# Performance work log

Hardware: AMD Instinct MI355X
Metric: run time of the kernel (lower is better)

The kernel has to match this reference:

```python
import jax, jax.numpy as jnp
import numpy as np

N_ENT = 200000
N_REL = 500
D_MODEL = 512
BS = 256


def setup_inputs() -> dict:
    key = jax.random.key(0)
    k1, k2, k3, k4, k5, k6 = jax.random.split(key, 6)
    return {
        "s_ent": jax.random.randint(k1, (BS,), 0, N_ENT, dtype=jnp.int32),
        "relation": jax.random.randint(k2, (BS,), 0, N_REL, dtype=jnp.int32),
        "o_ent": jax.random.randint(k3, (BS,), 0, N_ENT, dtype=jnp.int32),
        "time": jax.random.randint(k4, (BS,), 0, 365, dtype=jnp.int32),
        "ent_emb": jax.random.normal(k5, (N_ENT, D_MODEL), dtype=jnp.float32),
        "rel_emb": jax.random.normal(k6, (N_REL, D_MODEL), dtype=jnp.float32),
    }


def reference(s_ent, relation, o_ent, time, ent_emb, rel_emb):
    # test_forward: scores = -||(e_s + r) - E_all||_2 for every entity.
    # Faithful math via the ||a-b||^2 = ||a||^2 - 2 a.b + ||b||^2 GEMM
    # decomposition, avoiding the [bs, n_ent, d] difference tensor.
    cond = ent_emb[s_ent] + rel_emb[relation]          # [bs, d]
    a2 = jnp.sum(cond * cond, axis=-1, keepdims=True)  # [bs, 1]
    b2 = jnp.sum(ent_emb * ent_emb, axis=-1)           # [n_ent]
    ab = jnp.einsum('bd,nd->bn', cond, ent_emb)        # [bs, n_ent]
    d2 = a2 - 2.0 * ab + b2[None, :]
    scores = -jnp.sqrt(jnp.maximum(d2, 1e-12))
    return scores
```

## Files before the change

kernel.cpp:

```cpp
#include <hip/hip_runtime.h>
#include <hip/hip_bf16.h>

typedef __attribute__((ext_vector_type(8))) short short8;
typedef __attribute__((ext_vector_type(4))) float f32x4;

#define D_MODEL 512
#define BN 128
#define NT 16
#define A_TILE 16384
#define B_TILE 8192

__device__ __forceinline__ void gload16(const void* g, void* l) {
    typedef const __attribute__((address_space(1))) unsigned GT;
    typedef __attribute__((address_space(3))) unsigned LT;
    __builtin_amdgcn_global_load_lds((GT*)g, (LT*)l, 16, 0, 0);
}

__device__ __forceinline__ short f2bf(float f) {
    unsigned u = __builtin_bit_cast(unsigned, f);
    unsigned r = (u + 0x7fffu + ((u >> 16) & 1u)) >> 16;
    return (short)r;
}

__device__ __forceinline__ short8 cvt8(const float4& a, const float4& b) {
    union { __hip_bfloat162 h[4]; short8 s; } u;
    u.h[0] = __float22bfloat162_rn(make_float2(a.x, a.y));
    u.h[1] = __float22bfloat162_rn(make_float2(a.z, a.w));
    u.h[2] = __float22bfloat162_rn(make_float2(b.x, b.y));
    u.h[3] = __float22bfloat162_rn(make_float2(b.z, b.w));
    return u.s;
}
__device__ __forceinline__ float ssq(const float4& a, const float4& b) {
    return a.x*a.x + a.y*a.y + a.z*a.z + a.w*a.w
         + b.x*b.x + b.y*b.y + b.z*b.z + b.w*b.w;
}

__global__ void prep_kernel(const int* __restrict__ s_ent, const int* __restrict__ rel,
                            const float* __restrict__ ent, const float* __restrict__ relemb,
                            short* __restrict__ condb, float* __restrict__ a2) {
    const int b = blockIdx.x;
    const int t = threadIdx.x;
    const float4 v = *(const float4*)(ent + (size_t)s_ent[b] * D_MODEL + t * 4);
    const float4 w = *(const float4*)(relemb + (size_t)rel[b] * D_MODEL + t * 4);
    float c0 = v.x + w.x, c1 = v.y + w.y, c2 = v.z + w.z, c3 = v.w + w.w;
    float sq = c0 * c0 + c1 * c1 + c2 * c2 + c3 * c3;

    short4 s;
    s.x = f2bf(c0); s.y = f2bf(c1); s.z = f2bf(c2); s.w = f2bf(c3);
    *(short4*)(condb + (size_t)b * D_MODEL + t * 4) = s;

    #pragma unroll
    for (int off = 1; off < 64; off <<= 1) sq += __shfl_xor(sq, off);
    __shared__ float red[2];
    if ((t & 63) == 0) red[t >> 6] = sq;
    __syncthreads();
    if (t == 0) a2[b] = red[0] + red[1];
}

__global__ __launch_bounds__(512, 4)
void score_kernel(const float* __restrict__ ent, const short* __restrict__ condb,
                  const float* __restrict__ a2, float* __restrict__ out, const int n_ent) {
    __shared__ __align__(16) unsigned char lds[2 * A_TILE + 2 * B_TILE];
    unsigned char* Al = lds;
    unsigned char* Bl = lds + 2 * A_TILE;

    const int tid  = threadIdx.x;
    const int lane = tid & 63;
    const int w    = tid >> 6, wm = w >> 1, wn = w & 1;
    const int lrow = lane & 15, g4 = lane >> 4;
    const int nbase = blockIdx.x * BN;

    const int p0 = tid * 16, p1 = p0 + 8192;
    const int ar0 = p0 >> 6, ar1 = p1 >> 6;
    const char* gA0 = (const char*)condb + ar0 * 1024 + ((p0 & 63) ^ ((ar0 & 3) << 4));
    const char* gA1 = (const char*)condb + ar1 * 1024 + ((p1 & 63) ^ ((ar1 & 3) << 4));

    const int sr = tid >> 2, sk = (tid & 3) * 8;
    const long long gr = min((long long)(nbase + sr), (long long)(n_ent - 1));
    const float* gB = ent + gr * D_MODEL + sk;
    const int bwoff = sr * 64 + ((sk * 2) ^ ((sr & 3) << 4));

    const int base_a = (wm * 64 + lrow) * 64 + ((g4 * 16) ^ ((lrow & 3) << 4));
    const int base_b = (wn * 64 + lrow) * 64 + ((g4 * 16) ^ ((lrow & 3) << 4));

    f32x4 acc[4][4] = {};
    float sq = 0.f;

    float4 rbA0 = *(const float4*)(gB);
    float4 rbA1 = *(const float4*)(gB + 4);
    float4 rbB0 = *(const float4*)(gB + 32);
    float4 rbB1 = *(const float4*)(gB + 36);
    gload16(gA0, Al + p0);
    gload16(gA1, Al + p1);
    sq += ssq(rbA0, rbA1);
    *(short8*)(Bl + bwoff) = cvt8(rbA0, rbA1);

#define KSTEP(T, CV0, CV1, LD0, LD1, DO_CVT, DO_LDB, DO_LDA)                              \
  {                                                                                        \
    asm volatile("s_waitcnt vmcnt(0)" ::: "memory");                                       \
    short8 cb;                                                                             \
    if (DO_CVT) { sq += ssq(CV0, CV1); cb = cvt8(CV0, CV1); }                              \
    asm volatile("s_waitcnt lgkmcnt(0)" ::: "memory");                                     \
    __builtin_amdgcn_s_barrier();                                                          \
    if (DO_LDB) { LD0 = *(const float4*)(gB + ((T) + 2) * 32);                             \
                  LD1 = *(const float4*)(gB + ((T) + 2) * 32 + 4); }                       \
    if (DO_LDA) { unsigned char* ad = Al + (((T) + 1) & 1) * A_TILE;                       \
                  gload16(gA0 + ((T) + 1) * 64, ad + p0);                                  \
                  gload16(gA1 + ((T) + 1) * 64, ad + p1); }                                \
    if (DO_CVT) *(short8*)(Bl + (((T) + 1) & 1) * B_TILE + bwoff) = cb;                    \
    const unsigned char* ab = Al + ((T) & 1) * A_TILE;                                     \
    const unsigned char* bb = Bl + ((T) & 1) * B_TILE;                                     \
    short8 af0 = *(const short8*)(ab + base_a);                                            \
    short8 af1 = *(const short8*)(ab + base_a + 1024);                                     \
    short8 af2 = *(const short8*)(ab + base_a + 2048);                                     \
    short8 af3 = *(const short8*)(ab + base_a + 3072);                                     \
    _Pragma("unroll")                                                                      \
    for (int fn = 0; fn < 4; ++fn) {                                                       \
      short8 bf = *(const short8*)(bb + base_b + fn * 1024);                               \
      acc[0][fn] = __builtin_amdgcn_mfma_f32_16x16x32_bf16(af0, bf, acc[0][fn], 0, 0, 0);  \
      acc[1][fn] = __builtin_amdgcn_mfma_f32_16x16x32_bf16(af1, bf, acc[1][fn], 0, 0, 0);  \
      acc[2][fn] = __builtin_amdgcn_mfma_f32_16x16x32_bf16(af2, bf, acc[2][fn], 0, 0, 0);  \
      acc[3][fn] = __builtin_amdgcn_mfma_f32_16x16x32_bf16(af3, bf, acc[3][fn], 0, 0, 0);  \
    }                                                                                      \
  }

    for (int tt = 0; tt < 14; tt += 2) {
        KSTEP(tt,     rbB0, rbB1, rbA0, rbA1, true,  true,  true)
        KSTEP(tt + 1, rbA0, rbA1, rbB0, rbB1, true,  true,  true)
    }
    KSTEP(14, rbB0, rbB1, rbA0, rbA1, true,  false, true)
    KSTEP(15, rbA0, rbA1, rbB0, rbB1, false, false, false)
#undef KSTEP

    sq += __shfl_xor(sq, 1);
    sq += __shfl_xor(sq, 2);
    float* b2s = (float*)lds;
    if ((tid & 3) == 0) b2s[sr] = sq;
    __syncthreads();

    #pragma unroll
    for (int fm = 0; fm < 4; ++fm) {
        const int m0 = wm * 64 + fm * 16 + g4 * 4;
        const f32x4 a2v = *(const f32x4*)(a2 + m0);
        #pragma unroll
        for (int fn = 0; fn < 4; ++fn) {
            const int nl = wn * 64 + fn * 16 + lrow;
            const int ng = nbase + nl;
            if (ng < n_ent) {
                const float b2v = b2s[nl];
                #pragma unroll
                for (int r = 0; r < 4; ++r) {
                    float d2 = a2v[r] - 2.f * acc[fm][fn][r] + b2v;
                    out[(size_t)(m0 + r) * n_ent + ng] = -sqrtf(fmaxf(d2, 1e-12f));
                }
            }
        }
    }
}

extern "C" void kernel_launch(void* const* d_in, const int* in_sizes, int n_in,
                              void* d_out, int out_size, void* d_ws, size_t ws_size,
                              hipStream_t stream) {
    const int*   s_ent  = (const int*)d_in[0];
    const int*   rel    = (const int*)d_in[1];
    const float* ent    = (const float*)d_in[4];
    const float* relemb = (const float*)d_in[5];
    float* out = (float*)d_out;

    const int bs    = in_sizes[0];
    const int n_ent = in_sizes[4] / D_MODEL;

    short* condb = (short*)d_ws;
    float* a2    = (float*)((char*)d_ws + (size_t)bs * D_MODEL * 2);

    prep_kernel<<<bs, 128, 0, stream>>>(s_ent, rel, ent, relemb, condb, a2);

    const int ntiles = (n_ent + BN - 1) / BN;
    score_kernel<<<ntiles, 512, 0, stream>>>(ent, condb, a2, out, n_ent);
}
```

Baseline: 173.7 us.

## Deepen score kernel to triple-buffered pipeline with partial vmcnt waits and setprio

Switches the GEMM K-loop from double to triple buffering in LDS, with global loads issued two steps ahead. Waits now use partial vmcnt counts instead of draining all loads, so memory latency can overlap more compute. MFMA sections are wrapped in s_setprio to favour math issue. LDS per block grows, which may reduce the number of resident blocks per CU.

```diff
diff --git a/kernel.cpp b/kernel.cpp
--- a/kernel.cpp
+++ b/kernel.cpp
@@ -60,9 +60,9 @@
 __global__ __launch_bounds__(512, 4)
 void score_kernel(const float* __restrict__ ent, const short* __restrict__ condb,
                   const float* __restrict__ a2, float* __restrict__ out, const int n_ent) {
-    __shared__ __align__(16) unsigned char lds[2 * A_TILE + 2 * B_TILE];
+    __shared__ __align__(16) unsigned char lds[3 * A_TILE + 3 * B_TILE];
     unsigned char* Al = lds;
-    unsigned char* Bl = lds + 2 * A_TILE;
+    unsigned char* Bl = lds + 3 * A_TILE;
 
     const int tid  = threadIdx.x;
     const int lane = tid & 63;
@@ -86,34 +86,41 @@
     f32x4 acc[4][4] = {};
     float sq = 0.f;
 
-    float4 rbA0 = *(const float4*)(gB);
-    float4 rbA1 = *(const float4*)(gB + 4);
-    float4 rbB0 = *(const float4*)(gB + 32);
-    float4 rbB1 = *(const float4*)(gB + 36);
+    float4 rbE0 = *(const float4*)(gB);
+    float4 rbE1 = *(const float4*)(gB + 4);
+    asm volatile("s_waitcnt vmcnt(0)" ::: "memory");
+    sq += ssq(rbE0, rbE1);
+    *(short8*)(Bl + bwoff) = cvt8(rbE0, rbE1);
+    float4 rbO0 = *(const float4*)(gB + 32);
+    float4 rbO1 = *(const float4*)(gB + 36);
     gload16(gA0, Al + p0);
     gload16(gA1, Al + p1);
-    sq += ssq(rbA0, rbA1);
-    *(short8*)(Bl + bwoff) = cvt8(rbA0, rbA1);
+    rbE0 = *(const float4*)(gB + 64);
+    rbE1 = *(const float4*)(gB + 68);
+    gload16(gA0 + 64, Al + A_TILE + p0);
+    gload16(gA1 + 64, Al + A_TILE + p1);
 
-#define KSTEP(T, CV0, CV1, LD0, LD1, DO_CVT, DO_LDB, DO_LDA)                              \
+#define KSTEP(T, CV0, CV1, DO_CVT, DO_B, DO_A, VM)                                        \
   {                                                                                        \
-    asm volatile("s_waitcnt vmcnt(0)" ::: "memory");                                       \
-    short8 cb;                                                                             \
-    if (DO_CVT) { sq += ssq(CV0, CV1); cb = cvt8(CV0, CV1); }                              \
+    asm volatile("s_waitcnt vmcnt(" #VM ")" ::: "memory");                                 \
     asm volatile("s_waitcnt lgkmcnt(0)" ::: "memory");                                     \
     __builtin_amdgcn_s_barrier();                                                          \
-    if (DO_LDB) { LD0 = *(const float4*)(gB + ((T) + 2) * 32);                             \
-                  LD1 = *(const float4*)(gB + ((T) + 2) * 32 + 4); }                       \
-    if (DO_LDA) { unsigned char* ad = Al + (((T) + 1) & 1) * A_TILE;                       \
-                  gload16(gA0 + ((T) + 1) * 64, ad + p0);                                  \
-                  gload16(gA1 + ((T) + 1) * 64, ad + p1); }                                \
-    if (DO_CVT) *(short8*)(Bl + (((T) + 1) & 1) * B_TILE + bwoff) = cb;                    \
-    const unsigned char* ab = Al + ((T) & 1) * A_TILE;                                     \
-    const unsigned char* bb = Bl + ((T) & 1) * B_TILE;                                     \
+    if (DO_CVT) {                                                                          \
+      sq += ssq(CV0, CV1);                                                                 \
+      *(short8*)(Bl + (((T) + 1) % 3) * B_TILE + bwoff) = cvt8(CV0, CV1);                  \
+    }                                                                                      \
+    if (DO_B) { CV0 = *(const float4*)(gB + ((T) + 3) * 32);                               \
+                CV1 = *(const float4*)(gB + ((T) + 3) * 32 + 4); }                         \
+    if (DO_A) { unsigned char* ad = Al + (((T) + 2) % 3) * A_TILE;                         \
+                gload16(gA0 + ((T) + 2) * 64, ad + p0);                                    \
+                gload16(gA1 + ((T) + 2) * 64, ad + p1); }                                  \
+    const unsigned char* ab = Al + ((T) % 3) * A_TILE;                                     \
+    const unsigned char* bb = Bl + ((T) % 3) * B_TILE;                                     \
     short8 af0 = *(const short8*)(ab + base_a);                                            \
     short8 af1 = *(const short8*)(ab + base_a + 1024);                                     \
     short8 af2 = *(const short8*)(ab + base_a + 2048);                                     \
     short8 af3 = *(const short8*)(ab + base_a + 3072);                                     \
+    __builtin_amdgcn_s_setprio(1);                                                         \
     _Pragma("unroll")                                                                      \
     for (int fn = 0; fn < 4; ++fn) {                                                       \
       short8 bf = *(const short8*)(bb + base_b + fn * 1024);                               \
@@ -122,19 +129,30 @@
       acc[2][fn] = __builtin_amdgcn_mfma_f32_16x16x32_bf16(af2, bf, acc[2][fn], 0, 0, 0);  \
       acc[3][fn] = __builtin_amdgcn_mfma_f32_16x16x32_bf16(af3, bf, acc[3][fn], 0, 0, 0);  \
     }                                                                                      \
+    __builtin_amdgcn_s_setprio(0);                                                         \
   }
 
-    for (int tt = 0; tt < 14; tt += 2) {
-        KSTEP(tt,     rbB0, rbB1, rbA0, rbA1, true,  true,  true)
-        KSTEP(tt + 1, rbA0, rbA1, rbB0, rbB1, true,  true,  true)
-    }
-    KSTEP(14, rbB0, rbB1, rbA0, rbA1, true,  false, true)
-    KSTEP(15, rbA0, rbA1, rbB0, rbB1, false, false, false)
+    KSTEP(0,  rbO0, rbO1, true, true, true, 4)
+    KSTEP(1,  rbE0, rbE1, true, true, true, 4)
+    KSTEP(2,  rbO0, rbO1, true, true, true, 4)
+    KSTEP(3,  rbE0, rbE1, true, true, true, 4)
+    KSTEP(4,  rbO0, rbO1, true, true, true, 4)
+    KSTEP(5,  rbE0, rbE1, true, true, true, 4)
+    KSTEP(6,  rbO0, rbO1, true, true, true, 4)
+    KSTEP(7,  rbE0, rbE1, true, true, true, 4)
+    KSTEP(8,  rbO0, rbO1, true, true, true, 4)
+    KSTEP(9,  rbE0, rbE1, true, true, true, 4)
+    KSTEP(10, rbO0, rbO1, true, true, true, 4)
+    KSTEP(11, rbE0, rbE1, true, true, true, 4)
+    KSTEP(12, rbO0, rbO1, true,  true,  true,  4)
+    KSTEP(13, rbE0, rbE1, true,  false, true,  4)
+    KSTEP(14, rbO0, rbO1, true,  false, false, 2)
+    KSTEP(15, rbE0, rbE1, false, false, false, 0)
 #undef KSTEP
 
     sq += __shfl_xor(sq, 1);
     sq += __shfl_xor(sq, 2);
-    float* b2s = (float*)lds;
+    float* b2s = (float*)(lds + A_TILE);
     if ((tid & 3) == 0) b2s[sr] = sq;
     __syncthreads();
 
```

Measured after the change: 191.3 us. +10.2%, slower.
